# Kernel optimization log

Measured on AMD Instinct MI355X. Metric: run time of the kernel, lower is better.

Reference implementation:

```python
import jax, jax.numpy as jnp
import numpy as np

PATCH_SIZE = 16
MASK_RATIO = 0.35


def setup_inputs() -> dict:
    key = jax.random.key(0)
    kx, km = jax.random.split(key)
    B, C, H, W = 64, 3, 512, 512
    x = jax.random.normal(kx, (B, C, H, W), dtype=jnp.float32)
    # One Bernoulli decision per (batch, patch_row, patch_col); keep if rand >= mask_ratio
    u = jax.random.uniform(km, (B, H // PATCH_SIZE, W // PATCH_SIZE))
    keep_mask = u >= MASK_RATIO  # bool [B, 32, 32]
    return {"x": x, "keep_mask": keep_mask}


def reference(x, keep_mask):
    # Upsample patch-level keep mask to pixel resolution and apply in one
    # elementwise pass (equivalent to zeroing masked 16x16 patches).
    m = jnp.repeat(jnp.repeat(keep_mask, PATCH_SIZE, axis=1), PATCH_SIZE, axis=2)  # [B,H,W]
    return x * m[:, None, :, :].astype(x.dtype)
```

## Files before the change

kernel.cpp:

```cpp
#include <hip/hip_runtime.h>


#define W_DIM 512
#define H_DIM 512
#define CH 3
#define PATCH 16

__global__ __launch_bounds__(256) void PatchMask_kernel(
    const float4* __restrict__ x,
    const int* __restrict__ mask,
    float4* __restrict__ out,
    int n4)
{
    int i = blockIdx.x * blockDim.x + threadIdx.x;
    if (i >= n4) return;

    int e = i << 2;
    int w = e & (W_DIM - 1);
    int h = (e >> 9) & (H_DIM - 1);
    int bc = e >> 18;
    int b = bc / CH;

    int mi = (b << 10) + ((h >> 4) << 5) + (w >> 4);

    float4 v = x[i];
    if (mask[mi] == 0) {
        v.x = 0.f; v.y = 0.f; v.z = 0.f; v.w = 0.f;
    }
    out[i] = v;
}

extern "C" void kernel_launch(void* const* d_in, const int* in_sizes, int n_in,
                              void* d_out, int out_size, void* d_ws, size_t ws_size,
                              hipStream_t stream) {
    const float4* x   = (const float4*)d_in[0];
    const int* mask   = (const int*)d_in[1];
    float4* out       = (float4*)d_out;

    int n4 = out_size >> 2;
    int block = 256;
    int grid = (n4 + block - 1) / block;

    PatchMask_kernel<<<grid, block, 0, stream>>>(x, mask, out, n4);
}
```

Measured before the change: 320.8 us.

## Map one wave per patch and skip input loads for masked patches

Restructures the kernel so each 64-lane wave processes one 16x16 patch, reading the patch mask once via a wave-uniform index. Masked patches write zeros without loading x, reducing global read traffic. The tradeoff is less contiguous access: each wave touches sixteen 64-byte row segments strided across the image rather than one contiguous 1KB span.

```diff
diff --git a/kernel.cpp b/kernel.cpp
--- a/kernel.cpp
+++ b/kernel.cpp
@@ -1,33 +1,37 @@
 #include <hip/hip_runtime.h>
 
 
-#define W_DIM 512
-#define H_DIM 512
 #define CH 3
-#define PATCH 16
+#define WAVES_PER_BLOCK 4
 
 __global__ __launch_bounds__(256) void PatchMask_kernel(
     const float4* __restrict__ x,
     const int* __restrict__ mask,
     float4* __restrict__ out,
-    int n4)
+    int npatch)
 {
-    int i = blockIdx.x * blockDim.x + threadIdx.x;
-    if (i >= n4) return;
+    int lane = threadIdx.x & 63;
+    int p = blockIdx.x * WAVES_PER_BLOCK + (threadIdx.x >> 6);
+    if (p >= npatch) return;
 
-    int e = i << 2;
-    int w = e & (W_DIM - 1);
-    int h = (e >> 9) & (H_DIM - 1);
-    int bc = e >> 18;
-    int b = bc / CH;
+    int bc = p >> 10;
+    int pr = (p >> 5) & 31;
+    int pc = p & 31;
+    int b  = bc / CH;
 
-    int mi = (b << 10) + ((h >> 4) << 5) + (w >> 4);
+    int mi = __builtin_amdgcn_readfirstlane((b << 10) + (pr << 5) + pc);
+    int m  = mask[mi];
 
-    float4 v = x[i];
-    if (mask[mi] == 0) {
-        v.x = 0.f; v.y = 0.f; v.z = 0.f; v.w = 0.f;
+    int row = lane >> 2;
+    int c4  = lane & 3;
+    int i4 = (bc << 16) + (((pr << 4) + row) << 7) + (pc << 2) + c4;
+
+    if (m == 0) {
+        float4 z; z.x = 0.f; z.y = 0.f; z.z = 0.f; z.w = 0.f;
+        out[i4] = z;
+    } else {
+        out[i4] = x[i4];
     }
-    out[i] = v;
 }
 
 extern "C" void kernel_launch(void* const* d_in, const int* in_sizes, int n_in,
@@ -37,9 +41,9 @@
     const int* mask   = (const int*)d_in[1];
     float4* out       = (float4*)d_out;
 
-    int n4 = out_size >> 2;
-    int block = 256;
-    int grid = (n4 + block - 1) / block;
+    int npatch = out_size >> 8;
+    int block  = 256;
+    int grid   = (npatch + WAVES_PER_BLOCK - 1) / WAVES_PER_BLOCK;
 
-    PatchMask_kernel<<<grid, block, 0, stream>>>(x, mask, out, n4);
+    PatchMask_kernel<<<grid, block, 0, stream>>>(x, mask, out, npatch);
 }
```

After: 328.3 us. +2.4%, slower.
